# Kernel tuning notes

Measured on AMD Instinct MI355X. Metric: run time of the kernel, lower is better.

## Reference

```python
import jax, jax.numpy as jnp
import numpy as np

MARGIN = 0.2
PRED_RATE = 1.0
MAX_VIOLATION = True


def t2i_score(images, obj_nums, captions, cap_lens):
    """images: (Bi, O, D); captions: (Bc, W, D).
    For each image, keep only its first obj_nums[i] objects, compute all
    object-word similarities vs every caption, max-pool over objects,
    sum over all W words (incl. padding, as in the torch code), and
    normalize by caption length. Returns (Bi, Bc)."""
    O = images.shape[1]
    # dot[i, c, o, w] = <images[i, o], captions[c, w]>
    dot = jnp.einsum('iod,cwd->icow', images, captions)
    valid = jnp.arange(O)[None, :] < obj_nums[:, None]          # (Bi, O)
    dot = jnp.where(valid[:, None, :, None], dot, -jnp.inf)
    pooled = dot.max(axis=2).sum(axis=2)                        # (Bi, Bc)
    return pooled / cap_lens.astype(pooled.dtype)[None, :]


def setup_inputs() -> dict:
    key = jax.random.key(0)
    ks = jax.random.split(key, 10)
    B, O, W, D = 128, 36, 50, 128
    Op, Wp = 25, 30
    return {
        'im':         jax.random.normal(ks[0], (B, O, D), dtype=jnp.float32),
        'im_l':       jax.random.randint(ks[1], (B,), 1, O + 1, dtype=jnp.int32),
        's':          jax.random.normal(ks[2], (B, W, D), dtype=jnp.float32),
        's_l':        jax.random.randint(ks[3], (B,), 1, W + 1, dtype=jnp.int32),
        'pred':       jax.random.normal(ks[4], (B, Op, D), dtype=jnp.float32),
        'pred_l':     jax.random.randint(ks[5], (B,), 1, Op + 1, dtype=jnp.int32),
        'cap_o_pred': jax.random.normal(ks[6], (B, Op, D), dtype=jnp.float32),
        'cap_o_l':    jax.random.randint(ks[7], (B,), 1, Op + 1, dtype=jnp.int32),
        'c_r_pred':   jax.random.normal(ks[8], (B, Wp, D), dtype=jnp.float32),
        'c_r_l':      jax.random.randint(ks[9], (B,), 1, Wp + 1, dtype=jnp.int32),
    }


def reference(im, im_l, s, s_l, pred, pred_l, cap_o_pred, cap_o_l, c_r_pred, c_r_l):
    scores = (t2i_score(im, im_l, s, s_l)
              + PRED_RATE * t2i_score(pred, pred_l, c_r_pred, c_r_l))  # (B, B)
    B = scores.shape[0]
    diag = jnp.diagonal(scores)
    cost_s = jnp.maximum(MARGIN + scores - diag[:, None], 0.0)
    cost_im = jnp.maximum(MARGIN + scores - diag[None, :], 0.0)
    eye = jnp.eye(B, dtype=bool)
    cost_s = jnp.where(eye, 0.0, cost_s)
    cost_im = jnp.where(eye, 0.0, cost_im)
    if MAX_VIOLATION:
        cost_s = cost_s.max(axis=1)
        cost_im = cost_im.max(axis=0)
    return cost_s.sum() + cost_im.sum()
```

## Files before the change

### kernel.cpp

```cpp
#include <hip/hip_runtime.h>

typedef __bf16 bf16x8 __attribute__((ext_vector_type(8)));
typedef float f32x4 __attribute__((ext_vector_type(4)));
typedef unsigned int u32x4 __attribute__((ext_vector_type(4)));

__device__ __forceinline__ unsigned short f2bf(float f) {
  unsigned int u = __float_as_uint(f);
  u += 0x7FFFu + ((u >> 16) & 1u);
  return (unsigned short)(u >> 16);
}

__device__ __forceinline__ bf16x8 load_frag(const unsigned short* p) {
  u32x4 v = *(const u32x4*)p;
  return __builtin_bit_cast(bf16x8, v);
}

__global__ __launch_bounds__(256) void convert_all(
    const float* __restrict__ im, const float* __restrict__ s,
    const float* __restrict__ pred, const float* __restrict__ crp,
    unsigned short* __restrict__ imb, unsigned short* __restrict__ sb,
    unsigned short* __restrict__ pb, unsigned short* __restrict__ cb)
{
  int b = blockIdx.x;
  const float* src; unsigned short* dst; int O, OP, base;
  if (b < 768)       { src = im;   dst = imb; O = 36; OP = 48; base = 0; }
  else if (b < 1568) { src = s;    dst = sb;  O = 50; OP = 50; base = 768; }
  else if (b < 2080) { src = pred; dst = pb;  O = 25; OP = 32; base = 1568; }
  else               { src = crp;  dst = cb;  O = 30; OP = 30; base = 2080; }
  int tid = (b - base) * 256 + (int)threadIdx.x;
  int total = 128 * OP * 32;
  if (tid >= total) return;
  int d4 = tid & 31;
  int o  = (tid >> 5) % OP;
  int bb = tid / (OP * 32);
  unsigned short r0 = 0, r1 = 0, r2 = 0, r3 = 0;
  if (o < O) {
    const float4 v = *(const float4*)(src + ((bb * O + o) << 7) + (d4 << 2));
    r0 = f2bf(v.x); r1 = f2bf(v.y); r2 = f2bf(v.z); r3 = f2bf(v.w);
  }
  ushort4 outv; outv.x = r0; outv.y = r1; outv.z = r2; outv.w = r3;
  *(ushort4*)(dst + (size_t)tid * 4) = outv;
}

template<int MT, int W>
__device__ __forceinline__ void t2i_im2(
    const unsigned short* __restrict__ A,
    const unsigned short* __restrict__ Bw,
    const int* __restrict__ obj_l, const int* __restrict__ cap_l,
    float* __restrict__ pooled,
    int vb, float* wmax)
{
  const int ig  = vb >> 3;
  const int i0  = ig * 2;
  const int cg0 = (vb & 7) * 16;
  const int tid = threadIdx.x;
  const int wv = tid >> 6, lane = tid & 63;
  const int quad = lane >> 4, n16 = lane & 15;
  const int ol0 = obj_l[i0], ol1 = obj_l[i0 + 1];

  bf16x8 af[2][MT][4];
#pragma unroll
  for (int im = 0; im < 2; ++im) {
    const unsigned short* Ab =
        A + (((size_t)(i0 + im) * (MT * 16) + n16) << 7) + quad * 8;
#pragma unroll
    for (int t = 0; t < MT; ++t)
#pragma unroll
      for (int s = 0; s < 4; ++s)
        af[im][t][s] = load_frag(Ab + ((t * 16) << 7) + s * 32);
  }

  const unsigned short* Bbase = Bw + (((size_t)cg0 * W + n16) << 7) + quad * 8;

  for (int nt = wv; nt < W; nt += 4) {
    const unsigned short* bp = Bbase + ((nt * 16) << 7);
    bf16x8 bfrag[4];
#pragma unroll
    for (int s = 0; s < 4; ++s) bfrag[s] = load_frag(bp + s * 32);

    f32x4 acc[2][MT];
#pragma unroll
    for (int im = 0; im < 2; ++im)
#pragma unroll
      for (int t = 0; t < MT; ++t) { f32x4 z = {0.f,0.f,0.f,0.f}; acc[im][t] = z; }
#pragma unroll
    for (int s = 0; s < 4; ++s)
#pragma unroll
      for (int im = 0; im < 2; ++im)
#pragma unroll
        for (int t = 0; t < MT; ++t)
          acc[im][t] = __builtin_amdgcn_mfma_f32_16x16x32_bf16(
              af[im][t][s], bfrag[s], acc[im][t], 0, 0, 0);

#pragma unroll
    for (int im = 0; im < 2; ++im) {
      const int ol = im ? ol1 : ol0;
      float m = -3.0e38f;
#pragma unroll
      for (int t = 0; t < MT; ++t)
#pragma unroll
        for (int r = 0; r < 4; ++r) {
          int o = t * 16 + quad * 4 + r;
          if (o < ol) m = fmaxf(m, acc[im][t][r]);
        }
      m = fmaxf(m, __shfl_xor(m, 16));
      m = fmaxf(m, __shfl_xor(m, 32));
      if (quad == 0) wmax[im * (16 * W) + nt * 16 + n16] = m;
    }
  }
  __syncthreads();

  if (tid < 32) {
    const int im = tid >> 4, c = tid & 15;
    const float* wp = wmax + im * (16 * W) + c * W;
    float ssum = 0.f;
    for (int w = 0; w < W; ++w) ssum += wp[w];
    const int cc = cg0 + c;
    pooled[((i0 + im) << 7) + cc] = ssum / (float)cap_l[cc];
  }
}

__global__ __launch_bounds__(256) void t2i_both(
    const unsigned short* __restrict__ imb, const unsigned short* __restrict__ sb,
    const unsigned short* __restrict__ pb,  const unsigned short* __restrict__ cb,
    const int* __restrict__ im_l, const int* __restrict__ s_l,
    const int* __restrict__ pred_l, const int* __restrict__ crl,
    float* __restrict__ p1, float* __restrict__ p2)
{
  __shared__ float wmax[2 * 16 * 50];
  if (blockIdx.x < 512) t2i_im2<3, 50>(imb, sb, im_l, s_l, p1, blockIdx.x, wmax);
  else                  t2i_im2<2, 30>(pb, cb, pred_l, crl, p2, blockIdx.x - 512, wmax);
}

__global__ __launch_bounds__(1024) void loss_kernel(
    const float* __restrict__ p1, const float* __restrict__ p2,
    float* __restrict__ out)
{
  __shared__ float diag[128];
  __shared__ int   rowmaxi[128];
  __shared__ float colmax[8][128];
  __shared__ float wred[16];
  const int tid = threadIdx.x;
  const int sub = tid >> 7, j = tid & 127;
  if (sub == 0) {
    diag[j] = p1[j * 129] + p2[j * 129];
    rowmaxi[j] = 0;
  }
  __syncthreads();

  float colp = 0.f;
#pragma unroll
  for (int rr = 0; rr < 16; ++rr) {
    const int row = sub * 16 + rr;
    const float sc = p1[row * 128 + j] + p2[row * 128 + j];
    const float dr = diag[row];
    float rh = (j == row) ? 0.f : fmaxf(0.2f + sc - dr, 0.f);
    const float ch = (j == row) ? 0.f : fmaxf(0.2f + sc - diag[j], 0.f);
    colp = fmaxf(colp, ch);
#pragma unroll
    for (int o = 32; o; o >>= 1) rh = fmaxf(rh, __shfl_xor(rh, o));
    if ((tid & 63) == 0) atomicMax(&rowmaxi[row], __float_as_int(rh));
  }
  colmax[sub][j] = colp;
  __syncthreads();
  if (sub < 4) colmax[sub][j] = fmaxf(colmax[sub][j], colmax[sub + 4][j]);
  __syncthreads();
  if (sub < 2) colmax[sub][j] = fmaxf(colmax[sub][j], colmax[sub + 2][j]);
  __syncthreads();
  if (sub < 1) colmax[0][j] = fmaxf(colmax[0][j], colmax[1][j]);
  __syncthreads();

  float v = 0.f;
  if (tid < 128)      v = __int_as_float(rowmaxi[tid]);
  else if (tid < 256) v = colmax[0][tid - 128];
#pragma unroll
  for (int o = 32; o; o >>= 1) v += __shfl_xor(v, o);
  if ((tid & 63) == 0) wred[tid >> 6] = v;
  __syncthreads();
  if (tid == 0) {
    float sfin = 0.f;
    for (int k = 0; k < 16; ++k) sfin += wred[k];
    out[0] = sfin;
  }
}

extern "C" void kernel_launch(void* const* d_in, const int* in_sizes, int n_in,
                              void* d_out, int out_size, void* d_ws, size_t ws_size,
                              hipStream_t stream)
{
  const float* im     = (const float*)d_in[0];
  const int*   im_l   = (const int*)  d_in[1];
  const float* s      = (const float*)d_in[2];
  const int*   s_l    = (const int*)  d_in[3];
  const float* pred   = (const float*)d_in[4];
  const int*   pred_l = (const int*)  d_in[5];
  const float* crp    = (const float*)d_in[8];
  const int*   crl    = (const int*)  d_in[9];

  char* ws = (char*)d_ws;
  const size_t off_imb = 0;
  const size_t off_sb  = off_imb + (size_t)128 * 48 * 128 * 2;
  const size_t off_pb  = off_sb  + (size_t)128 * 50 * 128 * 2;
  const size_t off_cb  = off_pb  + (size_t)128 * 32 * 128 * 2;
  const size_t off_p1  = off_cb  + (size_t)128 * 30 * 128 * 2;
  const size_t off_p2  = off_p1  + (size_t)128 * 128 * 4;

  unsigned short* imb = (unsigned short*)(ws + off_imb);
  unsigned short* sb  = (unsigned short*)(ws + off_sb);
  unsigned short* pb  = (unsigned short*)(ws + off_pb);
  unsigned short* cb  = (unsigned short*)(ws + off_cb);
  float* p1 = (float*)(ws + off_p1);
  float* p2 = (float*)(ws + off_p2);

  hipLaunchKernelGGL(convert_all, dim3(2560), dim3(256), 0, stream,
                     im, s, pred, crp, imb, sb, pb, cb);
  hipLaunchKernelGGL(t2i_both, dim3(1024), dim3(256), 0, stream,
                     imb, sb, pb, cb, im_l, s_l, pred_l, crl, p1, p2);
  hipLaunchKernelGGL(loss_kernel, dim3(1), dim3(1024), 0, stream,
                     p1, p2, (float*)d_out);
}
```

Before: 121.0 us.

## Fuse convert, similarity and loss into one cooperative kernel with grid syncs

Replaces the three separate launches (bf16 conversion, pooled similarity, loss) with a single cooperative kernel of 512 blocks that uses grid.sync between phases. Each block converts a slice of the inputs, then computes one tile of each of the two similarity problems, and block 0 computes the loss using a rewritten row/column max reduction staged in shared memory. This removes launch gaps and inter-kernel overhead at the cost of grid-wide barriers, a large shared-memory union, and reduced parallelism in the similarity and loss phases. If the cooperative launch fails, it falls back to the old three-kernel path.

```diff
diff --git a/kernel.cpp b/kernel.cpp
--- a/kernel.cpp
+++ b/kernel.cpp
@@ -1,4 +1,7 @@
 #include <hip/hip_runtime.h>
+#include <hip/hip_cooperative_groups.h>
+
+namespace cg = cooperative_groups;
 
 typedef __bf16 bf16x8 __attribute__((ext_vector_type(8)));
 typedef float f32x4 __attribute__((ext_vector_type(4)));
@@ -13,6 +16,187 @@
 __device__ __forceinline__ bf16x8 load_frag(const unsigned short* p) {
   u32x4 v = *(const u32x4*)p;
   return __builtin_bit_cast(bf16x8, v);
+}
+
+template<int O, int OP>
+__device__ __forceinline__ void conv_unit(const float* __restrict__ src,
+                                          unsigned short* __restrict__ dst,
+                                          int rel)
+{
+  const int d4 = rel & 31;
+  const int o  = (rel >> 5) % OP;
+  const int bb = rel / (OP * 32);
+  ushort4 outv; outv.x = 0; outv.y = 0; outv.z = 0; outv.w = 0;
+  if (o < O) {
+    const float4 v = *(const float4*)(src + ((bb * O + o) << 7) + (d4 << 2));
+    outv.x = f2bf(v.x); outv.y = f2bf(v.y); outv.z = f2bf(v.z); outv.w = f2bf(v.w);
+  }
+  *(ushort4*)(dst + (size_t)rel * 4) = outv;
+}
+
+template<int MT, int W>
+__device__ __forceinline__ void t2i_im2(
+    const unsigned short* __restrict__ A,
+    const unsigned short* __restrict__ Bw,
+    const int* __restrict__ obj_l, const int* __restrict__ cap_l,
+    float* __restrict__ pooled,
+    int vb, float* wmax)
+{
+  const int ig  = vb >> 3;
+  const int i0  = ig * 2;
+  const int cg0 = (vb & 7) * 16;
+  const int tid = threadIdx.x;
+  const int wv = tid >> 6, lane = tid & 63;
+  const int quad = lane >> 4, n16 = lane & 15;
+  const int ol0 = obj_l[i0], ol1 = obj_l[i0 + 1];
+
+  bf16x8 af[2][MT][4];
+#pragma unroll
+  for (int im = 0; im < 2; ++im) {
+    const unsigned short* Ab =
+        A + (((size_t)(i0 + im) * (MT * 16) + n16) << 7) + quad * 8;
+#pragma unroll
+    for (int t = 0; t < MT; ++t)
+#pragma unroll
+      for (int s = 0; s < 4; ++s)
+        af[im][t][s] = load_frag(Ab + ((t * 16) << 7) + s * 32);
+  }
+
+  const unsigned short* Bbase = Bw + (((size_t)cg0 * W + n16) << 7) + quad * 8;
+
+  for (int nt = wv; nt < W; nt += 4) {
+    const unsigned short* bp = Bbase + ((nt * 16) << 7);
+    bf16x8 bfrag[4];
+#pragma unroll
+    for (int s = 0; s < 4; ++s) bfrag[s] = load_frag(bp + s * 32);
+
+    f32x4 acc[2][MT];
+#pragma unroll
+    for (int im = 0; im < 2; ++im)
+#pragma unroll
+      for (int t = 0; t < MT; ++t) { f32x4 z = {0.f,0.f,0.f,0.f}; acc[im][t] = z; }
+#pragma unroll
+    for (int s = 0; s < 4; ++s)
+#pragma unroll
+      for (int im = 0; im < 2; ++im)
+#pragma unroll
+        for (int t = 0; t < MT; ++t)
+          acc[im][t] = __builtin_amdgcn_mfma_f32_16x16x32_bf16(
+              af[im][t][s], bfrag[s], acc[im][t], 0, 0, 0);
+
+#pragma unroll
+    for (int im = 0; im < 2; ++im) {
+      const int ol = im ? ol1 : ol0;
+      float m = -3.0e38f;
+#pragma unroll
+      for (int t = 0; t < MT; ++t)
+#pragma unroll
+        for (int r = 0; r < 4; ++r) {
+          int o = t * 16 + quad * 4 + r;
+          if (o < ol) m = fmaxf(m, acc[im][t][r]);
+        }
+      m = fmaxf(m, __shfl_xor(m, 16));
+      m = fmaxf(m, __shfl_xor(m, 32));
+      if (quad == 0) wmax[im * (16 * W) + nt * 16 + n16] = m;
+    }
+  }
+  __syncthreads();
+
+  if (tid < 32) {
+    const int im = tid >> 4, c = tid & 15;
+    const float* wp = wmax + im * (16 * W) + c * W;
+    float ssum = 0.f;
+    for (int w = 0; w < W; ++w) ssum += wp[w];
+    const int cc = cg0 + c;
+    pooled[((i0 + im) << 7) + cc] = ssum / (float)cap_l[cc];
+  }
+}
+
+__global__ __launch_bounds__(256, 2) void fused_all(
+    const float* __restrict__ im, const float* __restrict__ s,
+    const float* __restrict__ pred, const float* __restrict__ crp,
+    const int* __restrict__ im_l, const int* __restrict__ s_l,
+    const int* __restrict__ pred_l, const int* __restrict__ crl,
+    unsigned short* __restrict__ imb, unsigned short* __restrict__ sb,
+    unsigned short* __restrict__ pb,  unsigned short* __restrict__ cb,
+    float* __restrict__ p1, float* __restrict__ p2, float* __restrict__ out)
+{
+  __shared__ union {
+    float wmax[2 * 16 * 50];
+    struct {
+      float S[128][129];
+      float rmax[128][2];
+      float cmax[2][128];
+      float wsum[4];
+    } L;
+  } sh;
+
+  cg::grid_group grid = cg::this_grid();
+  const int tid = threadIdx.x;
+
+  {
+    const int base = (int)blockIdx.x * 1280 + tid;
+#pragma unroll
+    for (int k = 0; k < 5; ++k) {
+      const int u = base + k * 256;
+      if (u < 196608)      conv_unit<36, 48>(im,   imb, u);
+      else if (u < 401408) conv_unit<50, 50>(s,    sb,  u - 196608);
+      else if (u < 532480) conv_unit<25, 32>(pred, pb,  u - 401408);
+      else                 conv_unit<30, 30>(crp,  cb,  u - 532480);
+    }
+  }
+  __threadfence();
+  grid.sync();
+
+  t2i_im2<3, 50>(imb, sb, im_l, s_l, p1, (int)blockIdx.x, sh.wmax);
+  __syncthreads();
+  t2i_im2<2, 30>(pb, cb, pred_l, crl, p2, (int)blockIdx.x, sh.wmax);
+  __threadfence();
+  grid.sync();
+
+  if (blockIdx.x != 0) return;
+
+  const int h = tid >> 7, j = tid & 127;
+  for (int rr = 0; rr < 64; ++rr) {
+    const int row = h * 64 + rr;
+    sh.L.S[row][j] = p1[row * 128 + j] + p2[row * 128 + j];
+  }
+  __syncthreads();
+
+  {
+    const int row = tid >> 1, half = tid & 1;
+    float m = -3.0e38f;
+    for (int k = 0; k < 64; ++k) {
+      const int c = half * 64 + k;
+      const float vv = sh.L.S[row][c];
+      m = (c == row) ? m : fmaxf(m, vv);
+    }
+    sh.L.rmax[row][half] = m;
+  }
+  {
+    float m = -3.0e38f;
+    for (int rr = 0; rr < 64; ++rr) {
+      const int row = h * 64 + rr;
+      const float vv = sh.L.S[row][j];
+      m = (row == j) ? m : fmaxf(m, vv);
+    }
+    sh.L.cmax[h][j] = m;
+  }
+  __syncthreads();
+
+  float v = 0.f;
+  if (tid < 128) {
+    const float d  = sh.L.S[tid][tid];
+    const float rm = fmaxf(sh.L.rmax[tid][0], sh.L.rmax[tid][1]);
+    const float cm = fmaxf(sh.L.cmax[0][tid], sh.L.cmax[1][tid]);
+    v = fmaxf(0.2f + rm - d, 0.f) + fmaxf(0.2f + cm - d, 0.f);
+  }
+#pragma unroll
+  for (int o = 32; o; o >>= 1) v += __shfl_xor(v, o);
+  if ((tid & 63) == 0) sh.L.wsum[tid >> 6] = v;
+  __syncthreads();
+  if (tid == 0)
+    out[0] = sh.L.wsum[0] + sh.L.wsum[1] + sh.L.wsum[2] + sh.L.wsum[3];
 }
 
 __global__ __launch_bounds__(256) void convert_all(
@@ -42,84 +226,6 @@
   *(ushort4*)(dst + (size_t)tid * 4) = outv;
 }
 
-template<int MT, int W>
-__device__ __forceinline__ void t2i_im2(
-    const unsigned short* __restrict__ A,
-    const unsigned short* __restrict__ Bw,
-    const int* __restrict__ obj_l, const int* __restrict__ cap_l,
-    float* __restrict__ pooled,
-    int vb, float* wmax)
-{
-  const int ig  = vb >> 3;
-  const int i0  = ig * 2;
-  const int cg0 = (vb & 7) * 16;
-  const int tid = threadIdx.x;
-  const int wv = tid >> 6, lane = tid & 63;
-  const int quad = lane >> 4, n16 = lane & 15;
-  const int ol0 = obj_l[i0], ol1 = obj_l[i0 + 1];
-
-  bf16x8 af[2][MT][4];
-#pragma unroll
-  for (int im = 0; im < 2; ++im) {
-    const unsigned short* Ab =
-        A + (((size_t)(i0 + im) * (MT * 16) + n16) << 7) + quad * 8;
-#pragma unroll
-    for (int t = 0; t < MT; ++t)
-#pragma unroll
-      for (int s = 0; s < 4; ++s)
-        af[im][t][s] = load_frag(Ab + ((t * 16) << 7) + s * 32);
-  }
-
-  const unsigned short* Bbase = Bw + (((size_t)cg0 * W + n16) << 7) + quad * 8;
-
-  for (int nt = wv; nt < W; nt += 4) {
-    const unsigned short* bp = Bbase + ((nt * 16) << 7);
-    bf16x8 bfrag[4];
-#pragma unroll
-    for (int s = 0; s < 4; ++s) bfrag[s] = load_frag(bp + s * 32);
-
-    f32x4 acc[2][MT];
-#pragma unroll
-    for (int im = 0; im < 2; ++im)
-#pragma unroll
-      for (int t = 0; t < MT; ++t) { f32x4 z = {0.f,0.f,0.f,0.f}; acc[im][t] = z; }
-#pragma unroll
-    for (int s = 0; s < 4; ++s)
-#pragma unroll
-      for (int im = 0; im < 2; ++im)
-#pragma unroll
-        for (int t = 0; t < MT; ++t)
-          acc[im][t] = __builtin_amdgcn_mfma_f32_16x16x32_bf16(
-              af[im][t][s], bfrag[s], acc[im][t], 0, 0, 0);
-
-#pragma unroll
-    for (int im = 0; im < 2; ++im) {
-      const int ol = im ? ol1 : ol0;
-      float m = -3.0e38f;
-#pragma unroll
-      for (int t = 0; t < MT; ++t)
-#pragma unroll
-        for (int r = 0; r < 4; ++r) {
-          int o = t * 16 + quad * 4 + r;
-          if (o < ol) m = fmaxf(m, acc[im][t][r]);
-        }
-      m = fmaxf(m, __shfl_xor(m, 16));
-      m = fmaxf(m, __shfl_xor(m, 32));
-      if (quad == 0) wmax[im * (16 * W) + nt * 16 + n16] = m;
-    }
-  }
-  __syncthreads();
-
-  if (tid < 32) {
-    const int im = tid >> 4, c = tid & 15;
-    const float* wp = wmax + im * (16 * W) + c * W;
-    float ssum = 0.f;
-    for (int w = 0; w < W; ++w) ssum += wp[w];
-    const int cc = cg0 + c;
-    pooled[((i0 + im) << 7) + cc] = ssum / (float)cap_l[cc];
-  }
-}
-
 __global__ __launch_bounds__(256) void t2i_both(
     const unsigned short* __restrict__ imb, const unsigned short* __restrict__ sb,
     const unsigned short* __restrict__ pb,  const unsigned short* __restrict__ cb,
@@ -211,11 +317,24 @@
   unsigned short* cb  = (unsigned short*)(ws + off_cb);
   float* p1 = (float*)(ws + off_p1);
   float* p2 = (float*)(ws + off_p2);
-
-  hipLaunchKernelGGL(convert_all, dim3(2560), dim3(256), 0, stream,
-                     im, s, pred, crp, imb, sb, pb, cb);
-  hipLaunchKernelGGL(t2i_both, dim3(1024), dim3(256), 0, stream,
-                     imb, sb, pb, cb, im_l, s_l, pred_l, crl, p1, p2);
-  hipLaunchKernelGGL(loss_kernel, dim3(1), dim3(1024), 0, stream,
-                     p1, p2, (float*)d_out);
-}
+  float* outp = (float*)d_out;
+
+  void* args[] = {
+    (void*)&im, (void*)&s, (void*)&pred, (void*)&crp,
+    (void*)&im_l, (void*)&s_l, (void*)&pred_l, (void*)&crl,
+    (void*)&imb, (void*)&sb, (void*)&pb, (void*)&cb,
+    (void*)&p1, (void*)&p2, (void*)&outp
+  };
+  hipError_t e = hipLaunchCooperativeKernel((const void*)fused_all,
+                                            dim3(512), dim3(256),
+                                            args, 0, stream);
+  if (e != hipSuccess) {
+    (void)hipGetLastError();
+    hipLaunchKernelGGL(convert_all, dim3(2560), dim3(256), 0, stream,
+                       im, s, pred, crp, imb, sb, pb, cb);
+    hipLaunchKernelGGL(t2i_both, dim3(1024), dim3(256), 0, stream,
+                       imb, sb, pb, cb, im_l, s_l, pred_l, crl, p1, p2);
+    hipLaunchKernelGGL(loss_kernel, dim3(1), dim3(1024), 0, stream,
+                       p1, p2, (float*)d_out);
+  }
+}
```

Result: slower. 345.9 us (+185.9%).

## Fuse loss reduction into similarity kernel via last-block ticket

Applied to the files above, without the earlier changes.

Removes the separate single-block loss kernel and runs the loss in whichever similarity block finishes last, chosen by an atomic ticket that the conversion kernel resets. The loss math is also restated as a row max and column max of the scores minus the diagonal, so the per-element hinge computation and the shared-memory atomic max go away. This saves one kernel launch and its scheduling gap. In exchange the final reduction now runs on only 256 threads in one block and depends on correct memory fencing of p1 and p2 across blocks.

```diff
diff --git a/kernel.cpp b/kernel.cpp
--- a/kernel.cpp
+++ b/kernel.cpp
@@ -19,9 +19,11 @@
     const float* __restrict__ im, const float* __restrict__ s,
     const float* __restrict__ pred, const float* __restrict__ crp,
     unsigned short* __restrict__ imb, unsigned short* __restrict__ sb,
-    unsigned short* __restrict__ pb, unsigned short* __restrict__ cb)
+    unsigned short* __restrict__ pb, unsigned short* __restrict__ cb,
+    unsigned int* __restrict__ ticket)
 {
   int b = blockIdx.x;
+  if (b == 0 && threadIdx.x == 0) *ticket = 0u;
   const float* src; unsigned short* dst; int O, OP, base;
   if (b < 768)       { src = im;   dst = imb; O = 36; OP = 48; base = 0; }
   else if (b < 1568) { src = s;    dst = sb;  O = 50; OP = 50; base = 768; }
@@ -120,68 +122,74 @@
   }
 }
 
-__global__ __launch_bounds__(256) void t2i_both(
+__global__ __launch_bounds__(256) void t2i_both_loss(
     const unsigned short* __restrict__ imb, const unsigned short* __restrict__ sb,
     const unsigned short* __restrict__ pb,  const unsigned short* __restrict__ cb,
     const int* __restrict__ im_l, const int* __restrict__ s_l,
     const int* __restrict__ pred_l, const int* __restrict__ crl,
-    float* __restrict__ p1, float* __restrict__ p2)
-{
-  __shared__ float wmax[2 * 16 * 50];
-  if (blockIdx.x < 512) t2i_im2<3, 50>(imb, sb, im_l, s_l, p1, blockIdx.x, wmax);
-  else                  t2i_im2<2, 30>(pb, cb, pred_l, crl, p2, blockIdx.x - 512, wmax);
-}
-
-__global__ __launch_bounds__(1024) void loss_kernel(
-    const float* __restrict__ p1, const float* __restrict__ p2,
-    float* __restrict__ out)
-{
-  __shared__ float diag[128];
-  __shared__ int   rowmaxi[128];
-  __shared__ float colmax[8][128];
-  __shared__ float wred[16];
+    float* __restrict__ p1, float* __restrict__ p2,
+    unsigned int* __restrict__ ticket, float* __restrict__ out)
+{
+  __shared__ union {
+    float wmax[2 * 16 * 50];
+    struct {
+      float cmax[2][128];
+      float rmax[2][128];
+      float wsum[2];
+    } L;
+  } sh;
+  __shared__ unsigned int winflag;
+
   const int tid = threadIdx.x;
-  const int sub = tid >> 7, j = tid & 127;
-  if (sub == 0) {
-    diag[j] = p1[j * 129] + p2[j * 129];
-    rowmaxi[j] = 0;
-  }
-  __syncthreads();
-
-  float colp = 0.f;
-#pragma unroll
-  for (int rr = 0; rr < 16; ++rr) {
-    const int row = sub * 16 + rr;
-    const float sc = p1[row * 128 + j] + p2[row * 128 + j];
-    const float dr = diag[row];
-    float rh = (j == row) ? 0.f : fmaxf(0.2f + sc - dr, 0.f);
-    const float ch = (j == row) ? 0.f : fmaxf(0.2f + sc - diag[j], 0.f);
-    colp = fmaxf(colp, ch);
-#pragma unroll
-    for (int o = 32; o; o >>= 1) rh = fmaxf(rh, __shfl_xor(rh, o));
-    if ((tid & 63) == 0) atomicMax(&rowmaxi[row], __float_as_int(rh));
-  }
-  colmax[sub][j] = colp;
-  __syncthreads();
-  if (sub < 4) colmax[sub][j] = fmaxf(colmax[sub][j], colmax[sub + 4][j]);
-  __syncthreads();
-  if (sub < 2) colmax[sub][j] = fmaxf(colmax[sub][j], colmax[sub + 2][j]);
-  __syncthreads();
-  if (sub < 1) colmax[0][j] = fmaxf(colmax[0][j], colmax[1][j]);
+
+  if (blockIdx.x < 512) t2i_im2<3, 50>(imb, sb, im_l, s_l, p1, blockIdx.x, sh.wmax);
+  else                  t2i_im2<2, 30>(pb, cb, pred_l, crl, p2, blockIdx.x - 512, sh.wmax);
+
+  __syncthreads();
+  if (tid == 0) {
+    unsigned int old = __hip_atomic_fetch_add(ticket, 1u, __ATOMIC_ACQ_REL,
+                                              __HIP_MEMORY_SCOPE_AGENT);
+    winflag = (old == 1023u) ? 1u : 0u;
+  }
+  __syncthreads();
+  if (winflag == 0u) return;
+  __threadfence();
+
+  const int h = tid >> 7, j = tid & 127;
+
+  {
+    float cm = -3.0e38f;
+    for (int rr = 0; rr < 64; ++rr) {
+      const int row = h * 64 + rr;
+      const float v = p1[row * 128 + j] + p2[row * 128 + j];
+      cm = (row == j) ? cm : fmaxf(cm, v);
+    }
+    sh.L.cmax[h][j] = cm;
+  }
+  {
+    float rm = -3.0e38f;
+    for (int k = 0; k < 64; ++k) {
+      const int c = h * 64 + k;
+      const float v = p1[j * 128 + c] + p2[j * 128 + c];
+      rm = (c == j) ? rm : fmaxf(rm, v);
+    }
+    sh.L.rmax[h][j] = rm;
+  }
   __syncthreads();
 
   float v = 0.f;
-  if (tid < 128)      v = __int_as_float(rowmaxi[tid]);
-  else if (tid < 256) v = colmax[0][tid - 128];
+  if (tid < 128) {
+    const float d  = p1[tid * 129] + p2[tid * 129];
+    const float rm = fmaxf(sh.L.rmax[0][tid], sh.L.rmax[1][tid]);
+    const float cm = fmaxf(sh.L.cmax[0][tid], sh.L.cmax[1][tid]);
+    v = fmaxf(0.2f + rm - d, 0.f) + fmaxf(0.2f + cm - d, 0.f);
+  }
 #pragma unroll
   for (int o = 32; o; o >>= 1) v += __shfl_xor(v, o);
-  if ((tid & 63) == 0) wred[tid >> 6] = v;
-  __syncthreads();
-  if (tid == 0) {
-    float sfin = 0.f;
-    for (int k = 0; k < 16; ++k) sfin += wred[k];
-    out[0] = sfin;
-  }
+  if (tid == 0)  sh.L.wsum[0] = v;
+  if (tid == 64) sh.L.wsum[1] = v;
+  __syncthreads();
+  if (tid == 0) out[0] = sh.L.wsum[0] + sh.L.wsum[1];
 }
 
 extern "C" void kernel_launch(void* const* d_in, const int* in_sizes, int n_in,
@@ -204,6 +212,7 @@
   const size_t off_cb  = off_pb  + (size_t)128 * 32 * 128 * 2;
   const size_t off_p1  = off_cb  + (size_t)128 * 30 * 128 * 2;
   const size_t off_p2  = off_p1  + (size_t)128 * 128 * 4;
+  const size_t off_tk  = off_p2  + (size_t)128 * 128 * 4;
 
   unsigned short* imb = (unsigned short*)(ws + off_imb);
   unsigned short* sb  = (unsigned short*)(ws + off_sb);
@@ -211,11 +220,11 @@
   unsigned short* cb  = (unsigned short*)(ws + off_cb);
   float* p1 = (float*)(ws + off_p1);
   float* p2 = (float*)(ws + off_p2);
+  unsigned int* ticket = (unsigned int*)(ws + off_tk);
 
   hipLaunchKernelGGL(convert_all, dim3(2560), dim3(256), 0, stream,
-                     im, s, pred, crp, imb, sb, pb, cb);
-  hipLaunchKernelGGL(t2i_both, dim3(1024), dim3(256), 0, stream,
-                     imb, sb, pb, cb, im_l, s_l, pred_l, crl, p1, p2);
-  hipLaunchKernelGGL(loss_kernel, dim3(1), dim3(1024), 0, stream,
-                     p1, p2, (float*)d_out);
-}
+                     im, s, pred, crp, imb, sb, pb, cb, ticket);
+  hipLaunchKernelGGL(t2i_both_loss, dim3(1024), dim3(256), 0, stream,
+                     imb, sb, pb, cb, im_l, s_l, pred_l, crl,
+                     p1, p2, ticket, (float*)d_out);
+}
```

Result: slower. 155.3 us (+28.4%).
